# Optimization experiments

Measured on AMD Instinct MI355X. Metric: run time of the kernel, lower is better.

The kernel has to match this reference:

```python
import jax, jax.numpy as jnp
import numpy as np

N_NODES = 100000
N_EDGES = 400000
IN_DIM = 100
OUT_DIM = 200
NUM_STEPS = 4


def setup_inputs() -> dict:
    key = jax.random.key(0)
    ks = jax.random.split(key, 8)
    x = jax.random.normal(ks[0], (N_NODES, IN_DIM), dtype=jnp.float32)
    edge_index = jax.random.randint(ks[1], (2, N_EDGES), 0, N_NODES, dtype=jnp.int64)
    s = 0.05
    W = jax.random.normal(ks[2], (NUM_STEPS, OUT_DIM, OUT_DIM), dtype=jnp.float32) * s
    w_ih = jax.random.normal(ks[3], (3 * OUT_DIM, OUT_DIM), dtype=jnp.float32) * s
    w_hh = jax.random.normal(ks[4], (3 * OUT_DIM, OUT_DIM), dtype=jnp.float32) * s
    b_ih = jax.random.normal(ks[5], (3 * OUT_DIM,), dtype=jnp.float32) * s
    b_hh = jax.random.normal(ks[6], (3 * OUT_DIM,), dtype=jnp.float32) * s
    cls_w = jax.random.normal(ks[7], (2, OUT_DIM), dtype=jnp.float32) * s
    cls_b = jnp.zeros((2,), dtype=jnp.float32)
    return {"x": x, "W": W, "w_ih": w_ih, "w_hh": w_hh, "b_ih": b_ih,
            "b_hh": b_hh, "cls_w": cls_w, "cls_b": cls_b, "edge_index": edge_index}


def _gru_cell(a, h, w_ih, w_hh, b_ih, b_hh):
    # torch.nn.GRUCell math: input a, hidden h
    gi = a @ w_ih.T + b_ih          # [N, 3D]
    gh = h @ w_hh.T + b_hh          # [N, 3D]
    i_r, i_z, i_n = jnp.split(gi, 3, axis=1)
    h_r, h_z, h_n = jnp.split(gh, 3, axis=1)
    r = jax.nn.sigmoid(i_r + h_r)
    z = jax.nn.sigmoid(i_z + h_z)
    n = jnp.tanh(i_n + r * h_n)
    return (1.0 - z) * n + z * h


def reference(x, W, w_ih, w_hh, b_ih, b_hh, cls_w, cls_b, edge_index):
    N = x.shape[0]
    # GatedGraphConv pads input features with zeros up to out_channels
    h = jnp.pad(x, ((0, 0), (0, OUT_DIM - x.shape[1])))
    src, dst = edge_index[0], edge_index[1]
    for i in range(NUM_STEPS):
        m = h @ W[i]                                         # [N, D]
        aggr = jax.ops.segment_sum(m[src], dst, num_segments=N)  # scatter-add
        h = _gru_cell(aggr, h, w_ih, w_hh, b_ih, b_hh)
    out = jax.nn.relu(h)
    # global_max_pool with all-zero batch ids -> max over all nodes
    pooled = jnp.max(out, axis=0, keepdims=True)             # [1, D]
    logits = pooled @ cls_w.T + cls_b                        # [1, 2]
    return jax.nn.softmax(logits, axis=1)
```

## Files before the change

kernel.cpp:

```cpp
#include <hip/hip_runtime.h>
#include <hip/hip_bf16.h>
#include <math.h>

#define N_NODES 100000
#define N_PAD   100096
#define N_EDGES 400000
#define IN_DIM  100
#define D       200
#define DP      208
#define KP      224
#define NUM_STEPS 4

#define HALF_SHORTS   9728
#define STAGE_GROUPS  19
#define GCAP          512
#define WCHUNKS_PER_SJT 2432
#define WCONV_BLOCKS  494

typedef __attribute__((ext_vector_type(8))) short bfrag;
typedef __attribute__((ext_vector_type(4))) float facc;

__device__ short g_Wall[NUM_STEPS * 13 * 2 * HALF_SHORTS];
__device__ float g_bias[6 * DP];

__device__ __forceinline__ float fast_sigmoid(float x) {
    return __builtin_amdgcn_rcpf(1.0f + __expf(-x));
}
__device__ __forceinline__ float fast_tanh(float x) {
    return 2.0f * __builtin_amdgcn_rcpf(1.0f + __expf(-2.0f * x)) - 1.0f;
}
__device__ __forceinline__ float bf2f(short u) {
    unsigned int x = ((unsigned int)(unsigned short)u) << 16;
    return __uint_as_float(x);
}

__global__ __launch_bounds__(256) void wconv_kernel(const float* __restrict__ W,
                                                    const float* __restrict__ w_ih,
                                                    const float* __restrict__ w_hh,
                                                    const float* __restrict__ b_ih,
                                                    const float* __restrict__ b_hh) {
    if (blockIdx.x >= WCONV_BLOCKS) {
        int idx = (blockIdx.x - WCONV_BLOCKS) * 256 + threadIdx.x;
        if (idx < 6 * DP) {
            int g = idx / DP, j = idx % DP;
            float v = 0.0f;
            if (j < D) v = (g < 3) ? b_ih[g * 200 + j] : b_hh[(g - 3) * 200 + j];
            g_bias[idx] = v;
        }
        return;
    }
    int idx = blockIdx.x * 256 + threadIdx.x;
    short* out = g_Wall + (size_t)idx * 8;
    int s    = idx / (13 * WCHUNKS_PER_SJT);
    int rem  = idx % (13 * WCHUNKS_PER_SJT);
    int jt   = rem / WCHUNKS_PER_SJT;
    int r2   = rem % WCHUNKS_PER_SJT;
    int half = r2 / 1216;
    int c    = r2 % 1216;
    if (c >= 1200) {
        #pragma unroll
        for (int i = 0; i < 8; ++i) out[i] = 0;
        return;
    }
    int gg = c / 400, cc = c % 400;
    int t  = (cc < 384) ? (cc >> 6) : 6;
    int l  = (cc < 384) ? (cc & 63) : (cc - 384);
    int g  = half * 3 + gg;
    int j  = jt * 16 + (l & 15);
    int k0 = t * 32 + (l >> 4) * 8;
    float vals[8];
    if (g < 3) {
        const float* wr = (j < D) ? &w_ih[(size_t)(g * 200 + j) * D] : nullptr;
        #pragma unroll
        for (int i = 0; i < 8; ++i) vals[i] = 0.0f;
        if (wr) {
            #pragma unroll
            for (int i = 0; i < 8; ++i) {
                int k = k0 + i;
                if (k < D) {
                    const float* Wr = &W[(size_t)s * D * D + (size_t)k * D];
                    float acc = 0.0f;
                    #pragma unroll 4
                    for (int tt = 0; tt < D; ++tt) acc += wr[tt] * Wr[tt];
                    vals[i] = acc;
                }
            }
        }
    } else {
        #pragma unroll
        for (int i = 0; i < 8; ++i) {
            int k = k0 + i;
            vals[i] = (j < D && k < D) ? w_hh[((size_t)(g - 3) * 200 + j) * D + k] : 0.0f;
        }
    }
    #pragma unroll
    for (int i = 0; i < 8; ++i) {
        __hip_bfloat16 b = __float2bfloat16(vals[i]);
        out[i] = *reinterpret_cast<short*>(&b);
    }
}

__global__ void pad_kernel(const float* __restrict__ x, __hip_bfloat16* __restrict__ h) {
    int idx = blockIdx.x * 256 + threadIdx.x;
    int n = idx / KP, c = idx % KP;
    float v = (n < N_NODES && c < IN_DIM) ? x[n * IN_DIM + c] : 0.0f;
    h[idx] = __float2bfloat16(v);
}

__global__ void count_kernel(const int* __restrict__ dst, int* __restrict__ cnt) {
    int e = blockIdx.x * blockDim.x + threadIdx.x;
    if (e < N_EDGES) atomicAdd(&cnt[dst[e]], 1);
}

#define SCAN_B 1024
#define NB_SCAN ((N_NODES + SCAN_B - 1) / SCAN_B)
__global__ __launch_bounds__(SCAN_B) void scan1(const int* __restrict__ cnt,
                                                int* __restrict__ incl, int* __restrict__ bsum) {
    __shared__ int ws[16];
    int i = blockIdx.x * SCAN_B + threadIdx.x;
    int lane = threadIdx.x & 63, wid = threadIdx.x >> 6;
    int v = (i < N_NODES) ? cnt[i] : 0;
    int s = v;
    #pragma unroll
    for (int o = 1; o < 64; o <<= 1) {
        int t = __shfl_up(s, o, 64);
        if (lane >= o) s += t;
    }
    if (lane == 63) ws[wid] = s;
    __syncthreads();
    if (wid == 0) {
        int t = (lane < 16) ? ws[lane] : 0;
        #pragma unroll
        for (int o = 1; o < 16; o <<= 1) {
            int u = __shfl_up(t, o, 64);
            if (lane >= o) t += u;
        }
        if (lane < 16) ws[lane] = t;
    }
    __syncthreads();
    if (wid > 0) s += ws[wid - 1];
    if (i < N_NODES) incl[i] = s;
    if (threadIdx.x == SCAN_B - 1) bsum[blockIdx.x] = s;
}
__global__ void scan3(const int* __restrict__ cnt, const int* __restrict__ incl,
                      const int* __restrict__ bsum, int* __restrict__ off,
                      int* __restrict__ cursor) {
    __shared__ int sh[128];
    if (threadIdx.x < 128) sh[threadIdx.x] = (threadIdx.x < NB_SCAN) ? bsum[threadIdx.x] : 0;
    __syncthreads();
    for (int o = 1; o < 128; o <<= 1) {
        int t = (threadIdx.x >= o && threadIdx.x < 128) ? sh[threadIdx.x - o] : 0;
        __syncthreads();
        if (threadIdx.x < 128) sh[threadIdx.x] += t;
        __syncthreads();
    }
    int i = blockIdx.x * blockDim.x + threadIdx.x;
    if (i < N_NODES) {
        int b = i / SCAN_B;
        int pre = b ? sh[b - 1] : 0;
        int v = incl[i] - cnt[i] + pre;
        off[i] = v; cursor[i] = v;
    }
    if (i == 0) off[N_NODES] = N_EDGES;
}
__global__ void fill_kernel(const int* __restrict__ src, const int* __restrict__ dst,
                            int* __restrict__ cursor, int* __restrict__ esrc) {
    int e = blockIdx.x * blockDim.x + threadIdx.x;
    if (e < N_EDGES) {
        int pos = atomicAdd(&cursor[dst[e]], 1);
        esrc[pos] = src[e];
    }
}

__device__ __forceinline__ void stage_half(const short* __restrict__ gsrc,
                                           short* lds_dst, int wave, int lane) {
    #pragma unroll
    for (int g = wave; g < STAGE_GROUPS; g += 4) {
        __builtin_amdgcn_global_load_lds(
            (const __attribute__((address_space(1))) void*)(gsrc + g * 512 + lane * 8),
            (__attribute__((address_space(3))) void*)(lds_dst + g * 512),
            16, 0, 0);
    }
}

__device__ __forceinline__ bfrag bv_load(const short* Bcur, int g, int t, int lane) {
    if (t < 6) return *(const bfrag*)(Bcur + g * 3200 + t * 512 + lane * 8);
    bfrag z;
    #pragma unroll
    for (int i = 0; i < 8; ++i) z[i] = 0;
    if (lane < 16) z = *(const bfrag*)(Bcur + g * 3200 + 3072 + lane * 8);
    return z;
}

__global__ __launch_bounds__(256) void gather_kernel(const __hip_bfloat16* __restrict__ hcur,
                                                     __hip_bfloat16* __restrict__ Ascr,
                                                     const int* __restrict__ off,
                                                     const int* __restrict__ esrc) {
    __shared__ int EIdxAll[4 * GCAP];
    int tid = threadIdx.x;
    int lane = tid & 63, wave = tid >> 6;
    int wbase = blockIdx.x * 32 + wave * 8;
    int* EIdx = EIdxAll + wave * GCAP;

    int nlo = wbase < N_NODES ? wbase : N_NODES;
    int nhi = (wbase + 8) < N_NODES ? (wbase + 8) : N_NODES;
    int lo = off[nlo];
    int cntw = off[nhi] - lo;
    bool use_lds = (cntw <= GCAP);
    if (use_lds)
        for (int i = lane; i < cntw; i += 64) EIdx[i] = esrc[lo + i];

    int r4 = lane >> 4;
    int ck = lane & 15;
    int colA = ck * 8;
    int colB = colA + 128;
    bool sumB = (ck < 9);
    #pragma unroll
    for (int it = 0; it < 2; ++it) {
        int rr = it * 4 + r4;
        int n = wbase + rr;
        float a[8] = {0, 0, 0, 0, 0, 0, 0, 0};
        float b[8] = {0, 0, 0, 0, 0, 0, 0, 0};
        if (n < N_NODES) {
            int e0 = off[n] - lo, e1 = off[n + 1] - lo;
            int nb = (e1 - e0 + 3) >> 2;
            for (int bq = 0; bq < nb; ++bq) {
                int eb = e0 + bq * 4;
                int i0, i1, i2, i3;
                if (use_lds) {
                    i0 = EIdx[eb];
                    i1 = (eb + 1 < e1) ? EIdx[eb + 1] : N_NODES;
                    i2 = (eb + 2 < e1) ? EIdx[eb + 2] : N_NODES;
                    i3 = (eb + 3 < e1) ? EIdx[eb + 3] : N_NODES;
                } else {
                    i0 = esrc[lo + eb];
                    i1 = (eb + 1 < e1) ? esrc[lo + eb + 1] : N_NODES;
                    i2 = (eb + 2 < e1) ? esrc[lo + eb + 2] : N_NODES;
                    i3 = (eb + 3 < e1) ? esrc[lo + eb + 3] : N_NODES;
                }
                size_t s0 = (size_t)i0 * KP, s1 = (size_t)i1 * KP;
                size_t s2 = (size_t)i2 * KP, s3 = (size_t)i3 * KP;
                bfrag a0 = *(const bfrag*)(hcur + s0 + colA);
                bfrag a1 = *(const bfrag*)(hcur + s1 + colA);
                bfrag a2 = *(const bfrag*)(hcur + s2 + colA);
                bfrag a3 = *(const bfrag*)(hcur + s3 + colA);
                if (sumB) {
                    bfrag b0 = *(const bfrag*)(hcur + s0 + colB);
                    bfrag b1 = *(const bfrag*)(hcur + s1 + colB);
                    bfrag b2 = *(const bfrag*)(hcur + s2 + colB);
                    bfrag b3 = *(const bfrag*)(hcur + s3 + colB);
                    #pragma unroll
                    for (int q = 0; q < 8; ++q)
                        b[q] += (bf2f(b0[q]) + bf2f(b1[q])) + (bf2f(b2[q]) + bf2f(b3[q]));
                }
                #pragma unroll
                for (int q = 0; q < 8; ++q)
                    a[q] += (bf2f(a0[q]) + bf2f(a1[q])) + (bf2f(a2[q]) + bf2f(a3[q]));
            }
        }
        __hip_bfloat16 oa[8], ob[8];
        #pragma unroll
        for (int q = 0; q < 8; ++q) {
            oa[q] = __float2bfloat16(a[q]);
            ob[q] = __float2bfloat16(b[q]);
        }
        __hip_bfloat16* arow = Ascr + (size_t)n * KP;
        *(ushort4*)(arow + colA)     = *(const ushort4*)&oa[0];
        *(ushort4*)(arow + colA + 4) = *(const ushort4*)&oa[4];
        if (ck < 12) {
            *(ushort4*)(arow + colB)     = *(const ushort4*)&ob[0];
            *(ushort4*)(arow + colB + 4) = *(const ushort4*)&ob[4];
        }
    }
}

__global__ __launch_bounds__(256, 2) void gemm_gru(const __hip_bfloat16* __restrict__ hcur,
                                                   const __hip_bfloat16* __restrict__ Ascr,
                                                   __hip_bfloat16* __restrict__ hnext,
                                                   unsigned int* __restrict__ pooled,
                                                   int step) {
    __shared__ __align__(16) short Bs[2][HALF_SHORTS];
    __shared__ unsigned int pmax[DP];
    int tid = threadIdx.x;
    int lane = tid & 63, wave = tid >> 6;
    int mrow = lane & 15, kq = lane >> 4;
    int jcol = lane & 15;
    int rowq = (lane >> 4) * 4;
    bool dopool = (step == NUM_STEPS - 1);

    if (dopool) for (int c = tid; c < DP; c += 256) pmax[c] = 0u;

    const short* Wstep = g_Wall + (size_t)step * 13 * (2 * HALF_SHORTS);
    int wbase = blockIdx.x * 128 + wave * 32;

    stage_half(Wstep, &Bs[0][0], wave, lane);

    bfrag av[2][7], hv[2][7];
    #pragma unroll
    for (int p = 0; p < 2; ++p) {
        const __hip_bfloat16* arow = Ascr + (size_t)(wbase + p * 16 + mrow) * KP;
        #pragma unroll
        for (int t = 0; t < 7; ++t)
            av[p][t] = *(const bfrag*)(arow + t * 32 + kq * 8);
    }
    const __hip_bfloat16* hrow0 = hcur + (size_t)(wbase + mrow) * KP;
    const __hip_bfloat16* hrow1 = hrow0 + (size_t)16 * KP;
    #pragma unroll
    for (int t = 0; t < 7; ++t) {
        hv[0][t] = *(const bfrag*)(hrow0 + t * 32 + kq * 8);
        hv[1][t] = *(const bfrag*)(hrow1 + t * 32 + kq * 8);
    }

    facc acc[4][2];
    unsigned short hold_u[2][4];

    for (int hk = 0; hk < 26; ++hk) {
        __syncthreads();
        if (hk + 1 < 26)
            stage_half(Wstep + (size_t)(hk + 1) * HALF_SHORTS,
                       &Bs[(hk + 1) & 1][0], wave, lane);

        int jt = hk >> 1;
        int j = jt * 16 + jcol;
        const short* Bcur = &Bs[hk & 1][0];

        if ((hk & 1) == 0) {
            #pragma unroll
            for (int mf = 0; mf < 2; ++mf)
                #pragma unroll
                for (int r = 0; r < 4; ++r)
                    hold_u[mf][r] = *(const unsigned short*)
                        (hcur + (size_t)(wbase + mf * 16 + rowq + r) * KP + j);
            #pragma unroll
            for (int g = 0; g < 4; ++g)
                #pragma unroll
                for (int mf = 0; mf < 2; ++mf) acc[g][mf] = (facc)(0.0f);
            #pragma unroll
            for (int t = 0; t < 7; ++t) {
                bfrag bv[3];
                #pragma unroll
                for (int g = 0; g < 3; ++g) bv[g] = bv_load(Bcur, g, t, lane);
                #pragma unroll
                for (int g = 0; g < 3; ++g)
                    #pragma unroll
                    for (int mf = 0; mf < 2; ++mf)
                        acc[g][mf] = __builtin_amdgcn_mfma_f32_16x16x32_bf16(av[mf][t], bv[g], acc[g][mf], 0, 0, 0);
            }
        } else {
            #pragma unroll
            for (int t = 0; t < 7; ++t) {
                bfrag bv[3];
                #pragma unroll
                for (int g = 0; g < 3; ++g) bv[g] = bv_load(Bcur, g, t, lane);
                #pragma unroll
                for (int mf = 0; mf < 2; ++mf) {
                    acc[0][mf] = __builtin_amdgcn_mfma_f32_16x16x32_bf16(hv[mf][t], bv[0], acc[0][mf], 0, 0, 0);
                    acc[1][mf] = __builtin_amdgcn_mfma_f32_16x16x32_bf16(hv[mf][t], bv[1], acc[1][mf], 0, 0, 0);
                    acc[3][mf] = __builtin_amdgcn_mfma_f32_16x16x32_bf16(hv[mf][t], bv[2], acc[3][mf], 0, 0, 0);
                }
            }

            float tmax = 0.0f;
            if (j < D) {
                float bir = g_bias[j],          biz = g_bias[DP + j],     bin = g_bias[2 * DP + j];
                float bhr = g_bias[3 * DP + j], bhz = g_bias[4 * DP + j], bhn = g_bias[5 * DP + j];
                #pragma unroll
                for (int mf = 0; mf < 2; ++mf) {
                    int m0 = wbase + mf * 16 + rowq;
                    #pragma unroll
                    for (int r = 0; r < 4; ++r) {
                        int m = m0 + r;
                        if (m < N_NODES) {
                            float hold = bf2f((short)hold_u[mf][r]);
                            float rr = fast_sigmoid(acc[0][mf][r] + bir + bhr);
                            float zz = fast_sigmoid(acc[1][mf][r] + biz + bhz);
                            float nn = fast_tanh(acc[2][mf][r] + bin + rr * (acc[3][mf][r] + bhn));
                            float hv2 = (1.0f - zz) * nn + zz * hold;
                            hnext[(size_t)m * KP + j] = __float2bfloat16(hv2);
                            if (hv2 > tmax) tmax = hv2;
                        }
                    }
                }
                if (dopool) atomicMax(&pmax[j], __float_as_uint(tmax));
            }
        }
    }

    if (dopool) {
        __syncthreads();
        for (int c = tid; c < D; c += 256) atomicMax(&pooled[c], pmax[c]);
    }
}

__global__ void head_kernel(const unsigned int* __restrict__ pooled,
                            const float* __restrict__ cls_w,
                            const float* __restrict__ cls_b,
                            float* __restrict__ out) {
    if (threadIdx.x == 0) {
        float l0 = cls_b[0], l1 = cls_b[1];
        for (int d = 0; d < D; ++d) {
            float p = __uint_as_float(pooled[d]);
            l0 += p * cls_w[d];
            l1 += p * cls_w[D + d];
        }
        float mx = l0 > l1 ? l0 : l1;
        float e0 = expf(l0 - mx), e1 = expf(l1 - mx);
        out[0] = e0 / (e0 + e1);
        out[1] = e1 / (e0 + e1);
    }
}

extern "C" void kernel_launch(void* const* d_in, const int* in_sizes, int n_in,
                              void* d_out, int out_size, void* d_ws, size_t ws_size,
                              hipStream_t stream) {
    const float* x     = (const float*)d_in[0];
    const float* W     = (const float*)d_in[1];
    const float* w_ih  = (const float*)d_in[2];
    const float* w_hh  = (const float*)d_in[3];
    const float* b_ih  = (const float*)d_in[4];
    const float* b_hh  = (const float*)d_in[5];
    const float* cls_w = (const float*)d_in[6];
    const float* cls_b = (const float*)d_in[7];
    const int*   ei    = (const int*)d_in[8];
    const int* src = ei;
    const int* dst = ei + N_EDGES;

    const size_t ROWB = (size_t)N_PAD * KP;
    __hip_bfloat16* hA   = (__hip_bfloat16*)d_ws;
    __hip_bfloat16* hB   = hA + ROWB;
    __hip_bfloat16* Ascr = hB + ROWB;
    int* cnt    = (int*)(Ascr + ROWB);
    int* incl   = cnt + N_NODES;
    int* bsum   = incl + N_NODES;
    int* off    = bsum + 128;
    int* cursor = off + N_NODES + 1;
    int* esrc   = cursor + N_NODES;
    unsigned int* pooled = (unsigned int*)(esrc + N_EDGES);

    hipMemsetAsync(cnt, 0, N_NODES * sizeof(int), stream);
    count_kernel<<<(N_EDGES + 255) / 256, 256, 0, stream>>>(dst, cnt);
    scan1<<<NB_SCAN, SCAN_B, 0, stream>>>(cnt, incl, bsum);
    scan3<<<(N_NODES + 255) / 256, 256, 0, stream>>>(cnt, incl, bsum, off, cursor);
    fill_kernel<<<(N_EDGES + 255) / 256, 256, 0, stream>>>(src, dst, cursor, esrc);

    wconv_kernel<<<WCONV_BLOCKS + 5, 256, 0, stream>>>(W, w_ih, w_hh, b_ih, b_hh);

    pad_kernel<<<(int)(ROWB / 256), 256, 0, stream>>>(x, hA);
    hipMemsetAsync(hB, 0, ROWB * sizeof(__hip_bfloat16), stream);
    hipMemsetAsync(pooled, 0, D * sizeof(unsigned int), stream);

    __hip_bfloat16* hcur = hA;
    __hip_bfloat16* hnext = hB;
    for (int s = 0; s < NUM_STEPS; ++s) {
        gather_kernel<<<N_PAD / 32, 256, 0, stream>>>(hcur, Ascr, off, esrc);
        gemm_gru<<<N_PAD / 128, 256, 0, stream>>>(hcur, Ascr, hnext, pooled, s);
        __hip_bfloat16* t = hcur; hcur = hnext; hnext = t;
    }
    head_kernel<<<1, 64, 0, stream>>>(pooled, cls_w, cls_b, (float*)d_out);
}
```

Measured before the change: 861.2 us.

## Read GRU weight fragments directly from global memory instead of LDS staging

Removes the double-buffered LDS staging of weight tiles (global_load_lds plus a per-half-tile barrier) in the fused GEMM+GRU kernel. Each wave now loads B fragments straight from global memory, relying on L1/L2 caching of the small per-step weight set. This drops 26 block barriers and the shared-memory footprint, which may allow more resident waves. The cost is redundant global/cache traffic per wave and exposed load latency in front of the MFMAs.

```diff
diff --git a/kernel.cpp b/kernel.cpp
--- a/kernel.cpp
+++ b/kernel.cpp
@@ -12,7 +12,6 @@
 #define NUM_STEPS 4
 
 #define HALF_SHORTS   9728
-#define STAGE_GROUPS  19
 #define GCAP          512
 #define WCHUNKS_PER_SJT 2432
 #define WCONV_BLOCKS  494
@@ -169,17 +168,6 @@
     if (e < N_EDGES) {
         int pos = atomicAdd(&cursor[dst[e]], 1);
         esrc[pos] = src[e];
-    }
-}
-
-__device__ __forceinline__ void stage_half(const short* __restrict__ gsrc,
-                                           short* lds_dst, int wave, int lane) {
-    #pragma unroll
-    for (int g = wave; g < STAGE_GROUPS; g += 4) {
-        __builtin_amdgcn_global_load_lds(
-            (const __attribute__((address_space(1))) void*)(gsrc + g * 512 + lane * 8),
-            (__attribute__((address_space(3))) void*)(lds_dst + g * 512),
-            16, 0, 0);
     }
 }
 
@@ -279,7 +267,6 @@
                                                    __hip_bfloat16* __restrict__ hnext,
                                                    unsigned int* __restrict__ pooled,
                                                    int step) {
-    __shared__ __align__(16) short Bs[2][HALF_SHORTS];
     __shared__ unsigned int pmax[DP];
     int tid = threadIdx.x;
     int lane = tid & 63, wave = tid >> 6;
@@ -288,12 +275,13 @@
     int rowq = (lane >> 4) * 4;
     bool dopool = (step == NUM_STEPS - 1);
 
-    if (dopool) for (int c = tid; c < DP; c += 256) pmax[c] = 0u;
+    if (dopool) {
+        for (int c = tid; c < DP; c += 256) pmax[c] = 0u;
+        __syncthreads();
+    }
 
     const short* Wstep = g_Wall + (size_t)step * 13 * (2 * HALF_SHORTS);
     int wbase = blockIdx.x * 128 + wave * 32;
-
-    stage_half(Wstep, &Bs[0][0], wave, lane);
 
     bfrag av[2][7], hv[2][7];
     #pragma unroll
@@ -314,75 +302,68 @@
     facc acc[4][2];
     unsigned short hold_u[2][4];
 
-    for (int hk = 0; hk < 26; ++hk) {
-        __syncthreads();
-        if (hk + 1 < 26)
-            stage_half(Wstep + (size_t)(hk + 1) * HALF_SHORTS,
-                       &Bs[(hk + 1) & 1][0], wave, lane);
-
-        int jt = hk >> 1;
+    for (int jt = 0; jt < 13; ++jt) {
         int j = jt * 16 + jcol;
-        const short* Bcur = &Bs[hk & 1][0];
-
-        if ((hk & 1) == 0) {
-            #pragma unroll
-            for (int mf = 0; mf < 2; ++mf)
+        const short* Bgi = Wstep + (size_t)(2 * jt) * HALF_SHORTS;
+        const short* Bgh = Bgi + HALF_SHORTS;
+
+        #pragma unroll
+        for (int mf = 0; mf < 2; ++mf)
+            #pragma unroll
+            for (int r = 0; r < 4; ++r)
+                hold_u[mf][r] = *(const unsigned short*)
+                    (hcur + (size_t)(wbase + mf * 16 + rowq + r) * KP + j);
+        #pragma unroll
+        for (int g = 0; g < 4; ++g)
+            #pragma unroll
+            for (int mf = 0; mf < 2; ++mf) acc[g][mf] = (facc)(0.0f);
+
+        #pragma unroll
+        for (int t = 0; t < 7; ++t) {
+            bfrag bv[3];
+            #pragma unroll
+            for (int g = 0; g < 3; ++g) bv[g] = bv_load(Bgi, g, t, lane);
+            #pragma unroll
+            for (int g = 0; g < 3; ++g)
                 #pragma unroll
-                for (int r = 0; r < 4; ++r)
-                    hold_u[mf][r] = *(const unsigned short*)
-                        (hcur + (size_t)(wbase + mf * 16 + rowq + r) * KP + j);
-            #pragma unroll
-            for (int g = 0; g < 4; ++g)
+                for (int mf = 0; mf < 2; ++mf)
+                    acc[g][mf] = __builtin_amdgcn_mfma_f32_16x16x32_bf16(av[mf][t], bv[g], acc[g][mf], 0, 0, 0);
+        }
+        #pragma unroll
+        for (int t = 0; t < 7; ++t) {
+            bfrag bv[3];
+            #pragma unroll
+            for (int g = 0; g < 3; ++g) bv[g] = bv_load(Bgh, g, t, lane);
+            #pragma unroll
+            for (int mf = 0; mf < 2; ++mf) {
+                acc[0][mf] = __builtin_amdgcn_mfma_f32_16x16x32_bf16(hv[mf][t], bv[0], acc[0][mf], 0, 0, 0);
+                acc[1][mf] = __builtin_amdgcn_mfma_f32_16x16x32_bf16(hv[mf][t], bv[1], acc[1][mf], 0, 0, 0);
+                acc[3][mf] = __builtin_amdgcn_mfma_f32_16x16x32_bf16(hv[mf][t], bv[2], acc[3][mf], 0, 0, 0);
+            }
+        }
+
+        float tmax = 0.0f;
+        if (j < D) {
+            float bir = g_bias[j],          biz = g_bias[DP + j],     bin = g_bias[2 * DP + j];
+            float bhr = g_bias[3 * DP + j], bhz = g_bias[4 * DP + j], bhn = g_bias[5 * DP + j];
+            #pragma unroll
+            for (int mf = 0; mf < 2; ++mf) {
+                int m0 = wbase + mf * 16 + rowq;
                 #pragma unroll
-                for (int mf = 0; mf < 2; ++mf) acc[g][mf] = (facc)(0.0f);
-            #pragma unroll
-            for (int t = 0; t < 7; ++t) {
-                bfrag bv[3];
-                #pragma unroll
-                for (int g = 0; g < 3; ++g) bv[g] = bv_load(Bcur, g, t, lane);
-                #pragma unroll
-                for (int g = 0; g < 3; ++g)
-                    #pragma unroll
-                    for (int mf = 0; mf < 2; ++mf)
-                        acc[g][mf] = __builtin_amdgcn_mfma_f32_16x16x32_bf16(av[mf][t], bv[g], acc[g][mf], 0, 0, 0);
-            }
-        } else {
-            #pragma unroll
-            for (int t = 0; t < 7; ++t) {
-                bfrag bv[3];
-                #pragma unroll
-                for (int g = 0; g < 3; ++g) bv[g] = bv_load(Bcur, g, t, lane);
-                #pragma unroll
-                for (int mf = 0; mf < 2; ++mf) {
-                    acc[0][mf] = __builtin_amdgcn_mfma_f32_16x16x32_bf16(hv[mf][t], bv[0], acc[0][mf], 0, 0, 0);
-                    acc[1][mf] = __builtin_amdgcn_mfma_f32_16x16x32_bf16(hv[mf][t], bv[1], acc[1][mf], 0, 0, 0);
-                    acc[3][mf] = __builtin_amdgcn_mfma_f32_16x16x32_bf16(hv[mf][t], bv[2], acc[3][mf], 0, 0, 0);
+                for (int r = 0; r < 4; ++r) {
+                    int m = m0 + r;
+                    if (m < N_NODES) {
+                        float hold = bf2f((short)hold_u[mf][r]);
+                        float rr = fast_sigmoid(acc[0][mf][r] + bir + bhr);
+                        float zz = fast_sigmoid(acc[1][mf][r] + biz + bhz);
+                        float nn = fast_tanh(acc[2][mf][r] + bin + rr * (acc[3][mf][r] + bhn));
+                        float hv2 = (1.0f - zz) * nn + zz * hold;
+                        hnext[(size_t)m * KP + j] = __float2bfloat16(hv2);
+                        if (hv2 > tmax) tmax = hv2;
+                    }
                 }
             }
-
-            float tmax = 0.0f;
-            if (j < D) {
-                float bir = g_bias[j],          biz = g_bias[DP + j],     bin = g_bias[2 * DP + j];
-                float bhr = g_bias[3 * DP + j], bhz = g_bias[4 * DP + j], bhn = g_bias[5 * DP + j];
-                #pragma unroll
-                for (int mf = 0; mf < 2; ++mf) {
-                    int m0 = wbase + mf * 16 + rowq;
-                    #pragma unroll
-                    for (int r = 0; r < 4; ++r) {
-                        int m = m0 + r;
-                        if (m < N_NODES) {
-                            float hold = bf2f((short)hold_u[mf][r]);
-                            float rr = fast_sigmoid(acc[0][mf][r] + bir + bhr);
-                            float zz = fast_sigmoid(acc[1][mf][r] + biz + bhz);
-                            float nn = fast_tanh(acc[2][mf][r] + bin + rr * (acc[3][mf][r] + bhn));
-                            float hv2 = (1.0f - zz) * nn + zz * hold;
-                            hnext[(size_t)m * KP + j] = __float2bfloat16(hv2);
-                            if (hv2 > tmax) tmax = hv2;
-                        }
-                    }
-                }
-                if (dopool) atomicMax(&pmax[j], __float_as_uint(tmax));
-            }
+            if (dopool) atomicMax(&pmax[j], __float_as_uint(tmax));
         }
     }
 
```

Result: slower. 1.268 ms (+47.3%).
